# Kernel optimization log

Hardware: AMD Instinct MI355X
Metric: run time of the kernel (lower is better)

The kernel has to match this reference:

```python
import jax, jax.numpy as jnp
import numpy as np

HIDDEN = 1024
INTER = 2048
NUM_EXPERTS = 8
TOP_K = 2
GROUP_SIZE = 128
TOKENS = 4096


def _dequant_int4(packed, scale, group_size):
    # packed: [E, N, K//2] ints in [0,256) holding two uint4 nibbles (low | high<<4)
    # scale:  [E, N, K//group_size] float32
    E, N, Kh = packed.shape
    K = 2 * Kh
    low = packed & 0xF
    high = (packed >> 4) & 0xF
    # interleave: even K positions = low nibble, odd = high nibble
    q = jnp.stack([low, high], axis=-1).reshape(E, N, K) - 8  # int4 values in [-8,7]
    q = q.astype(jnp.float32).reshape(E, N, K // group_size, group_size)
    w = q * scale[..., None]
    return w.reshape(E, N, K)


def setup_inputs() -> dict:
    key = jax.random.key(0)
    k1, k2, k3, k4, k5, k6 = jax.random.split(key, 6)
    x = jax.random.normal(k1, (TOKENS, HIDDEN), dtype=jnp.float32)
    router_w = jax.random.normal(k2, (NUM_EXPERTS, HIDDEN), dtype=jnp.float32) * 0.02
    w1 = jax.random.randint(k3, (NUM_EXPERTS, 2 * INTER, HIDDEN // 2), 0, 256, dtype=jnp.int32)
    w1_scale = jax.random.uniform(k4, (NUM_EXPERTS, 2 * INTER, HIDDEN // GROUP_SIZE), dtype=jnp.float32) * 0.05
    w2 = jax.random.randint(k5, (NUM_EXPERTS, HIDDEN, INTER // 2), 0, 256, dtype=jnp.int32)
    w2_scale = jax.random.uniform(k6, (NUM_EXPERTS, HIDDEN, INTER // GROUP_SIZE), dtype=jnp.float32) * 0.05
    return {"x": x, "router_w": router_w, "w1": w1, "w1_scale": w1_scale, "w2": w2, "w2_scale": w2_scale}


def reference(x, router_w, w1, w1_scale, w2, w2_scale):
    # Router: topk then softmax over the top-k logits
    scores = x @ router_w.T                                 # [T, E]
    top_w, top_i = jax.lax.top_k(scores, TOP_K)             # [T, K]
    top_w = jax.nn.softmax(top_w, axis=-1).astype(jnp.float32)

    # Dequantize int4 grouped weights once
    w1_deq = _dequant_int4(w1, w1_scale, GROUP_SIZE)        # [E, 2I, H]
    w2_deq = _dequant_int4(w2, w2_scale, GROUP_SIZE)        # [E, H, I]

    out = jnp.zeros_like(x)
    for e in range(NUM_EXPERTS):
        # per-token routing weight for expert e (0 if not routed)
        ge = jnp.sum(top_w * (top_i == e), axis=-1)         # [T]
        h = x @ w1_deq[e].T                                  # [T, 2I]
        gate, up = h[:, :INTER], h[:, INTER:]
        a = jax.nn.silu(gate) * up                           # SwiGLU
        y = a @ w2_deq[e].T                                  # [T, H]
        out = out + ge[:, None] * y
    return out
```

## Files before the change

kernel.cpp:

```cpp
#include <hip/hip_runtime.h>
#include <hip/hip_bf16.h>

#define HIDDEN 1024
#define INTER 2048
#define NE 8
#define GS 128
#define TOKENS 4096
#define MAXROWS 9216
#define MAXTILES 72

typedef __bf16 bf16x8 __attribute__((ext_vector_type(8)));
typedef float f32x4 __attribute__((ext_vector_type(4)));

#define OFF_TOPKI 0u
#define OFF_TOPKW 32768u
#define OFF_CTRL  65536u
#define OFF_TOK   66048u
#define OFF_SLOT  102912u
#define OFF_TILE  135680u
#define OFF_XB    139776u
#define OFF_A     8530432u
#define OFF_W1D   46279168u
#define OFF_W2D   113388032u
#define OFF_Y0    OFF_W1D

__device__ __forceinline__ unsigned short f2bf(float f) {
  union { float f; unsigned int u; } v; v.f = f;
  unsigned int r = (v.u + 0x7FFFu + ((v.u >> 16) & 1u)) >> 16;
  return (unsigned short)r;
}
__device__ __forceinline__ float bf2f(unsigned int u) {
  union { unsigned int u; float f; } v; v.u = u << 16;
  return v.f;
}
__device__ __forceinline__ unsigned int pack2(unsigned short lo, unsigned short hi) {
  return (unsigned int)lo | ((unsigned int)hi << 16);
}

typedef const __attribute__((address_space(1))) unsigned int GAS;
typedef __attribute__((address_space(3))) unsigned int LAS;
__device__ __forceinline__ void gload16(const unsigned short* g, unsigned short* l) {
  __builtin_amdgcn_global_load_lds((GAS*)g, (LAS*)l, 16, 0, 0);
}


__global__ __launch_bounds__(256) void k_prep(const float* __restrict__ x,
    const float* __restrict__ rw, int* __restrict__ topki, float* __restrict__ topkw,
    const int* __restrict__ w1, const float* __restrict__ w1s,
    unsigned short* __restrict__ w1f,
    const int* __restrict__ w2, const float* __restrict__ w2s,
    unsigned short* __restrict__ w2f, unsigned short* __restrict__ xb) {
  int bid = blockIdx.x, tid = threadIdx.x;
  if (bid == 25600) {
    uint2 z; z.x = 0u; z.y = 0u;
    *reinterpret_cast<uint2*>(xb + (size_t)TOKENS * HIDDEN + tid * 4) = z;
    return;
  }
  if (bid >= 17408) {
    int gid = (bid - 17408) * 256 + tid;
    int lane = gid & 63, kt = (gid >> 6) & 63, ntP = (gid >> 12) & 63, e = gid >> 18;
    int n = ntP * 16 + (lane & 15), q = lane >> 4;
    size_t R = (size_t)e * 1024 + n;
    float s = w2s[R * 16 + (kt >> 2)];
    int4 p = *reinterpret_cast<const int4*>(w2 + R * 1024 + kt * 16 + q * 4);
    int pv[4] = { p.x, p.y, p.z, p.w };
    uint4 o; unsigned int ov[4];
#pragma unroll
    for (int j = 0; j < 4; j++) {
      float lo = (float)((pv[j] & 15) - 8) * s;
      float hi = (float)(((pv[j] >> 4) & 15) - 8) * s;
      ov[j] = pack2(f2bf(lo), f2bf(hi));
    }
    o.x = ov[0]; o.y = ov[1]; o.z = ov[2]; o.w = ov[3];
    *reinterpret_cast<uint4*>(w2f + (size_t)gid * 8) = o;
    return;
  }
  if (bid >= 1024) {
    int gid = (bid - 1024) * 256 + tid;
    int lane = gid & 63, kt = (gid >> 6) & 31, ntP = (gid >> 11) & 255, e = gid >> 19;
    int n = ntP * 16 + (lane & 15), q = lane >> 4;
    size_t R = (size_t)e * 4096 + n;
    float s = w1s[R * 8 + (kt >> 2)];
    int4 p = *reinterpret_cast<const int4*>(w1 + R * 512 + kt * 16 + q * 4);
    int pv[4] = { p.x, p.y, p.z, p.w };
    uint4 o; unsigned int ov[4];
#pragma unroll
    for (int j = 0; j < 4; j++) {
      float lo = (float)((pv[j] & 15) - 8) * s;
      float hi = (float)(((pv[j] >> 4) & 15) - 8) * s;
      ov[j] = pack2(f2bf(lo), f2bf(hi));
    }
    o.x = ov[0]; o.y = ov[1]; o.z = ov[2]; o.w = ov[3];
    *reinterpret_cast<uint4*>(w1f + (size_t)gid * 8) = o;
    return;
  }
  int wave = tid >> 6, lane = tid & 63;
  int t = bid * 4 + wave;
  float acc[NE];
#pragma unroll
  for (int e = 0; e < NE; e++) acc[e] = 0.f;
  const float* xr = x + (size_t)t * HIDDEN;
  unsigned short* xbr = xb + (size_t)t * HIDDEN;
  for (int i = lane; i < HIDDEN; i += 64) {
    float xv = xr[i];
    xbr[i] = f2bf(xv);
#pragma unroll
    for (int e = 0; e < NE; e++) acc[e] += xv * rw[e * HIDDEN + i];
  }
#pragma unroll
  for (int e = 0; e < NE; e++) {
    float v = acc[e];
    for (int off = 32; off > 0; off >>= 1) v += __shfl_down(v, off, 64);
    acc[e] = v;
  }
  if (lane == 0) {
    int b0 = 0; float s0 = acc[0];
#pragma unroll
    for (int e = 1; e < NE; e++) if (acc[e] > s0) { s0 = acc[e]; b0 = e; }
    int b1 = -1; float s1 = -3.0e38f;
#pragma unroll
    for (int e = 0; e < NE; e++) if (e != b0 && acc[e] > s1) { s1 = acc[e]; b1 = e; }
    float w0 = 1.f / (1.f + __expf(s1 - s0));
    topki[t * 2] = b0; topki[t * 2 + 1] = b1;
    topkw[t * 2] = w0; topkw[t * 2 + 1] = 1.f - w0;
  }
}

__global__ __launch_bounds__(256) void k_route2(const int* __restrict__ topki,
    int* __restrict__ ctrl, int* __restrict__ tok, int* __restrict__ slots,
    int* __restrict__ tilemap) {
  __shared__ int h[NE], off[NE], cnt[NE];
  int tid = threadIdx.x;
  if (tid < NE) h[tid] = 0;
  __syncthreads();
  for (int i = tid; i < TOKENS * 2; i += 256) atomicAdd(&h[topki[i]], 1);
  __syncthreads();
  if (tid == 0) {
    int run = 0, t = 0;
    for (int e = 0; e < NE; e++) {
      int c = h[e];
      ctrl[e] = c; ctrl[16 + e] = run; off[e] = run;
      int pc = (c + 127) & ~127;
      for (int mt = 0; mt < (pc >> 7); mt++) tilemap[t++] = (e << 20) | (run + mt * 128);
      run += pc;
    }
    ctrl[24] = run; ctrl[25] = t;
  }
  __syncthreads();
#pragma unroll
  for (int e = 0; e < NE; e++) {
    int c = h[e], pc = (c + 127) & ~127;
    for (int i = c + tid; i < pc; i += 256) tok[off[e] + i] = -1;
  }
  if (tid < NE) cnt[tid] = off[tid];
  __syncthreads();
  for (int i = tid; i < TOKENS * 2; i += 256) {
    int e = topki[i];
    int p = atomicAdd(&cnt[e], 1);
    tok[p] = i >> 1;
    slots[i] = p;
  }
}

__global__ __launch_bounds__(256) void k_gemm1(
    const unsigned short* __restrict__ xb, const unsigned short* __restrict__ w1f,
    const int* __restrict__ ctrl, const int* __restrict__ tilemap,
    const int* __restrict__ tok, unsigned short* __restrict__ a_f) {
  __shared__ unsigned short sA[128 * 32];
  int bid = blockIdx.x, tid = threadIdx.x;
  int nt = bid & 31, tile = bid >> 5;
  if (tile >= ctrl[25]) return;
  int tm = tilemap[tile];
  int e = tm >> 20, row0 = tm & 0xFFFFF;
  int wave = tid >> 6, lane = tid & 63;
  int ln = lane & 15, quad = lane >> 4;
  int wr = (wave & 1) * 64, wc = (wave >> 1) * 32;

  int srow = tid >> 2, scblk = tid & 3;
  int scol = (scblk ^ ((srow >> 1) & 3)) * 8;
  int t0 = tok[row0 + srow];
  int t1 = tok[row0 + 64 + srow];
  const unsigned short* gA0 = xb + (size_t)(t0 < 0 ? TOKENS : t0) * HIDDEN + scol;
  const unsigned short* gA1 = xb + (size_t)(t1 < 0 ? TOKENS : t1) * HIDDEN + scol;
  unsigned short* lA0 = sA + tid * 8;
  unsigned short* lA1 = sA + 64 * 32 + tid * 8;

  int ntPg = nt * 4 + (wave >> 1) * 2;
  const unsigned short* pbg0 = w1f + (size_t)(e * 256 + ntPg) * 16384 + lane * 8;
  const unsigned short* pbg1 = w1f + (size_t)(e * 256 + ntPg + 1) * 16384 + lane * 8;
  const unsigned short* pbu0 = w1f + (size_t)(e * 256 + 128 + ntPg) * 16384 + lane * 8;
  const unsigned short* pbu1 = w1f + (size_t)(e * 256 + 128 + ntPg + 1) * 16384 + lane * 8;

  bf16x8 bgc[2], buc[2];
  bgc[0] = *reinterpret_cast<const bf16x8*>(pbg0);
  bgc[1] = *reinterpret_cast<const bf16x8*>(pbg1);
  buc[0] = *reinterpret_cast<const bf16x8*>(pbu0);
  buc[1] = *reinterpret_cast<const bf16x8*>(pbu1);

  f32x4 aG[4][2] = {}, aU[4][2] = {};
#pragma unroll 2
  for (int kt = 0; kt < 32; kt++) {
    __syncthreads();
    gload16(gA0 + kt * 32, lA0);
    gload16(gA1 + kt * 32, lA1);
    __syncthreads();
    int o = (kt < 31) ? (kt + 1) * 512 : 0;
    bf16x8 bgn0 = *reinterpret_cast<const bf16x8*>(pbg0 + o);
    bf16x8 bgn1 = *reinterpret_cast<const bf16x8*>(pbg1 + o);
    bf16x8 bun0 = *reinterpret_cast<const bf16x8*>(pbu0 + o);
    bf16x8 bun1 = *reinterpret_cast<const bf16x8*>(pbu1 + o);
    bf16x8 af[4];
#pragma unroll
    for (int m = 0; m < 4; m++) {
      int ar = wr + m * 16 + ln;
      af[m] = *reinterpret_cast<const bf16x8*>(&sA[ar * 32 + (quad ^ ((ar >> 1) & 3)) * 8]);
    }
#pragma unroll
    for (int m = 0; m < 4; m++) {
      aG[m][0] = __builtin_amdgcn_mfma_f32_16x16x32_bf16(af[m], bgc[0], aG[m][0], 0, 0, 0);
      aG[m][1] = __builtin_amdgcn_mfma_f32_16x16x32_bf16(af[m], bgc[1], aG[m][1], 0, 0, 0);
      aU[m][0] = __builtin_amdgcn_mfma_f32_16x16x32_bf16(af[m], buc[0], aU[m][0], 0, 0, 0);
      aU[m][1] = __builtin_amdgcn_mfma_f32_16x16x32_bf16(af[m], buc[1], aU[m][1], 0, 0, 0);
    }
    bgc[0] = bgn0; bgc[1] = bgn1; buc[0] = bun0; buc[1] = bun1;
  }
#pragma unroll
  for (int m = 0; m < 4; m++)
#pragma unroll
    for (int n = 0; n < 2; n++) {
      int c = nt * 64 + wc + n * 16 + ln;
      int kta = c >> 5, qa = (c >> 3) & 3, ja = c & 7;
#pragma unroll
      for (int r = 0; r < 4; r++) {
        float g = aG[m][n][r], u = aU[m][n][r];
        float act = (g / (1.f + __expf(-g))) * u;
        int row = row0 + wr + m * 16 + quad * 4 + r;
        size_t idx = ((size_t)((row >> 4) * 64 + kta) * 64 + qa * 16 + (row & 15)) * 8 + ja;
        a_f[idx] = f2bf(act);
      }
    }
}

__global__ __launch_bounds__(256) void k_gemm2(
    const unsigned short* __restrict__ a_f, const unsigned short* __restrict__ w2f,
    const int* __restrict__ ctrl, const int* __restrict__ tilemap,
    unsigned short* __restrict__ y) {
  int bid = blockIdx.x, tid = threadIdx.x;
  int kp = bid & 1, nt = (bid >> 1) & 7, tile = bid >> 4;
  if (tile >= ctrl[25]) return;
  int tm = tilemap[tile];
  int e = tm >> 20, row0 = tm & 0xFFFFF;
  int n0 = nt * 128;
  int wave = tid >> 6, lane = tid & 63;
  int ln = lane & 15, quad = lane >> 4;
  int wr = (wave & 1) * 64, wc = (wave >> 1) * 64;

  int rt0 = (row0 >> 4) + (wave & 1) * 4;
  int ntP0 = nt * 8 + (wave >> 1) * 4;
  const unsigned short* pa[4];
  const unsigned short* pb[4];
#pragma unroll
  for (int m = 0; m < 4; m++)
    pa[m] = a_f + ((size_t)(rt0 + m) * 64 + kp * 32) * 512 + lane * 8;
#pragma unroll
  for (int n = 0; n < 4; n++)
    pb[n] = w2f + ((size_t)(e * 64 + ntP0 + n) * 64 + kp * 32) * 512 + lane * 8;

  bf16x8 ac[4], bc[4];
#pragma unroll
  for (int m = 0; m < 4; m++) ac[m] = *reinterpret_cast<const bf16x8*>(pa[m]);
#pragma unroll
  for (int n = 0; n < 4; n++) bc[n] = *reinterpret_cast<const bf16x8*>(pb[n]);

  f32x4 acc[4][4] = {};
#pragma unroll 2
  for (int i = 0; i < 32; i++) {
    int o = (i < 31) ? (i + 1) * 512 : 0;
    bf16x8 an[4], bn[4];
#pragma unroll
    for (int m = 0; m < 4; m++) an[m] = *reinterpret_cast<const bf16x8*>(pa[m] + o);
#pragma unroll
    for (int n = 0; n < 4; n++) bn[n] = *reinterpret_cast<const bf16x8*>(pb[n] + o);
#pragma unroll
    for (int m = 0; m < 4; m++)
#pragma unroll
      for (int n = 0; n < 4; n++)
        acc[m][n] = __builtin_amdgcn_mfma_f32_16x16x32_bf16(ac[m], bc[n], acc[m][n], 0, 0, 0);
#pragma unroll
    for (int m = 0; m < 4; m++) ac[m] = an[m];
#pragma unroll
    for (int n = 0; n < 4; n++) bc[n] = bn[n];
  }
  unsigned short* yk = y + (size_t)kp * MAXROWS * HIDDEN;
#pragma unroll
  for (int m = 0; m < 4; m++)
#pragma unroll
    for (int n = 0; n < 4; n++) {
      int col = n0 + wc + n * 16 + ln;
#pragma unroll
      for (int r = 0; r < 4; r++) {
        int row = row0 + wr + m * 16 + quad * 4 + r;
        yk[(size_t)row * HIDDEN + col] = f2bf(acc[m][n][r]);
      }
    }
}

__global__ __launch_bounds__(256) void k_combine(const unsigned short* __restrict__ y,
    const int* __restrict__ slots, const float* __restrict__ topkw,
    float* __restrict__ out) {
  int t = blockIdx.x;
  int c = threadIdx.x * 4;
  int s0 = slots[t * 2], s1 = slots[t * 2 + 1];
  float g0 = topkw[t * 2], g1 = topkw[t * 2 + 1];
  const unsigned short* y1 = y + (size_t)MAXROWS * HIDDEN;
  uint2 a0 = *reinterpret_cast<const uint2*>(y  + (size_t)s0 * HIDDEN + c);
  uint2 a1 = *reinterpret_cast<const uint2*>(y1 + (size_t)s0 * HIDDEN + c);
  uint2 b0 = *reinterpret_cast<const uint2*>(y  + (size_t)s1 * HIDDEN + c);
  uint2 b1 = *reinterpret_cast<const uint2*>(y1 + (size_t)s1 * HIDDEN + c);
  float4 o;
  o.x = g0 * (bf2f(a0.x & 0xffffu) + bf2f(a1.x & 0xffffu))
      + g1 * (bf2f(b0.x & 0xffffu) + bf2f(b1.x & 0xffffu));
  o.y = g0 * (bf2f(a0.x >> 16) + bf2f(a1.x >> 16))
      + g1 * (bf2f(b0.x >> 16) + bf2f(b1.x >> 16));
  o.z = g0 * (bf2f(a0.y & 0xffffu) + bf2f(a1.y & 0xffffu))
      + g1 * (bf2f(b0.y & 0xffffu) + bf2f(b1.y & 0xffffu));
  o.w = g0 * (bf2f(a0.y >> 16) + bf2f(a1.y >> 16))
      + g1 * (bf2f(b0.y >> 16) + bf2f(b1.y >> 16));
  *reinterpret_cast<float4*>(out + (size_t)t * HIDDEN + c) = o;
}

extern "C" void kernel_launch(void* const* d_in, const int* in_sizes, int n_in,
                              void* d_out, int out_size, void* d_ws, size_t ws_size,
                              hipStream_t stream) {
  const float* x   = (const float*)d_in[0];
  const float* rw  = (const float*)d_in[1];
  const int*   w1  = (const int*)d_in[2];
  const float* w1s = (const float*)d_in[3];
  const int*   w2  = (const int*)d_in[4];
  const float* w2s = (const float*)d_in[5];
  float* out = (float*)d_out;
  char* ws = (char*)d_ws;

  int*   topki = (int*)(ws + OFF_TOPKI);
  float* topkw = (float*)(ws + OFF_TOPKW);
  int*   ctrl  = (int*)(ws + OFF_CTRL);
  int*   tok   = (int*)(ws + OFF_TOK);
  int*   slots = (int*)(ws + OFF_SLOT);
  int*   tilemap = (int*)(ws + OFF_TILE);
  unsigned short* xb  = (unsigned short*)(ws + OFF_XB);
  unsigned short* a_f = (unsigned short*)(ws + OFF_A);
  unsigned short* w1f = (unsigned short*)(ws + OFF_W1D);
  unsigned short* w2f = (unsigned short*)(ws + OFF_W2D);
  unsigned short* y   = (unsigned short*)(ws + OFF_Y0);

  k_prep<<<25601, 256, 0, stream>>>(x, rw, topki, topkw, w1, w1s, w1f, w2, w2s, w2f, xb);
  k_route2<<<1, 256, 0, stream>>>(topki, ctrl, tok, slots, tilemap);
  k_gemm1<<<32 * MAXTILES, 256, 0, stream>>>(xb, w1f, ctrl, tilemap, tok, a_f);
  k_gemm2<<<16 * MAXTILES, 256, 0, stream>>>(a_f, w2f, ctrl, tilemap, y);
  k_combine<<<TOKENS, 256, 0, stream>>>(y, slots, topkw, out);
}
```

Baseline: 351.5 us.

## Stage gemm1 weights through LDS from row-major dequantized layout

The w1 dequant now writes a plain row-major [E, 2I, H] bf16 array with fully coalesced reads, instead of the MFMA-fragment-packed layout. gemm1 loads gate and up weight tiles into swizzled shared memory with global_load_lds, alongside the activation tile, and reads the B fragments from LDS. This removes the per-lane register prefetch of B fragments. It adds LDS traffic and loses the overlap of next-iteration weight loads with the MFMAs, since the loop is now fully synchronous with no double buffering.

```diff
diff --git a/kernel.cpp b/kernel.cpp
--- a/kernel.cpp
+++ b/kernel.cpp
@@ -47,7 +47,7 @@
 __global__ __launch_bounds__(256) void k_prep(const float* __restrict__ x,
     const float* __restrict__ rw, int* __restrict__ topki, float* __restrict__ topkw,
     const int* __restrict__ w1, const float* __restrict__ w1s,
-    unsigned short* __restrict__ w1f,
+    unsigned short* __restrict__ w1d,
     const int* __restrict__ w2, const float* __restrict__ w2s,
     unsigned short* __restrict__ w2f, unsigned short* __restrict__ xb) {
   int bid = blockIdx.x, tid = threadIdx.x;
@@ -77,11 +77,11 @@
   }
   if (bid >= 1024) {
     int gid = (bid - 1024) * 256 + tid;
-    int lane = gid & 63, kt = (gid >> 6) & 31, ntP = (gid >> 11) & 255, e = gid >> 19;
-    int n = ntP * 16 + (lane & 15), q = lane >> 4;
-    size_t R = (size_t)e * 4096 + n;
-    float s = w1s[R * 8 + (kt >> 2)];
-    int4 p = *reinterpret_cast<const int4*>(w1 + R * 512 + kt * 16 + q * 4);
+    int i4 = gid * 4;
+    int r = i4 >> 9;
+    int i = i4 & 511;
+    float s = w1s[r * 8 + (i >> 6)];
+    int4 p = *reinterpret_cast<const int4*>(w1 + (size_t)i4);
     int pv[4] = { p.x, p.y, p.z, p.w };
     uint4 o; unsigned int ov[4];
 #pragma unroll
@@ -91,7 +91,7 @@
       ov[j] = pack2(f2bf(lo), f2bf(hi));
     }
     o.x = ov[0]; o.y = ov[1]; o.z = ov[2]; o.w = ov[3];
-    *reinterpret_cast<uint4*>(w1f + (size_t)gid * 8) = o;
+    *reinterpret_cast<uint4*>(w1d + ((size_t)r << 10) + 2 * i) = o;
     return;
   }
   int wave = tid >> 6, lane = tid & 63;
@@ -163,15 +163,18 @@
 }
 
 __global__ __launch_bounds__(256) void k_gemm1(
-    const unsigned short* __restrict__ xb, const unsigned short* __restrict__ w1f,
+    const unsigned short* __restrict__ xb, const unsigned short* __restrict__ w1d,
     const int* __restrict__ ctrl, const int* __restrict__ tilemap,
     const int* __restrict__ tok, unsigned short* __restrict__ a_f) {
   __shared__ unsigned short sA[128 * 32];
+  __shared__ unsigned short sBg[64 * 32];
+  __shared__ unsigned short sBu[64 * 32];
   int bid = blockIdx.x, tid = threadIdx.x;
   int nt = bid & 31, tile = bid >> 5;
   if (tile >= ctrl[25]) return;
   int tm = tilemap[tile];
   int e = tm >> 20, row0 = tm & 0xFFFFF;
+  int n0 = nt * 64;
   int wave = tid >> 6, lane = tid & 63;
   int ln = lane & 15, quad = lane >> 4;
   int wr = (wave & 1) * 64, wc = (wave >> 1) * 32;
@@ -182,53 +185,47 @@
   int t1 = tok[row0 + 64 + srow];
   const unsigned short* gA0 = xb + (size_t)(t0 < 0 ? TOKENS : t0) * HIDDEN + scol;
   const unsigned short* gA1 = xb + (size_t)(t1 < 0 ? TOKENS : t1) * HIDDEN + scol;
+  const unsigned short* gBg = w1d + ((size_t)e * 4096 + n0 + srow) * HIDDEN + scol;
+  const unsigned short* gBu = gBg + (size_t)INTER * HIDDEN;
   unsigned short* lA0 = sA + tid * 8;
   unsigned short* lA1 = sA + 64 * 32 + tid * 8;
-
-  int ntPg = nt * 4 + (wave >> 1) * 2;
-  const unsigned short* pbg0 = w1f + (size_t)(e * 256 + ntPg) * 16384 + lane * 8;
-  const unsigned short* pbg1 = w1f + (size_t)(e * 256 + ntPg + 1) * 16384 + lane * 8;
-  const unsigned short* pbu0 = w1f + (size_t)(e * 256 + 128 + ntPg) * 16384 + lane * 8;
-  const unsigned short* pbu1 = w1f + (size_t)(e * 256 + 128 + ntPg + 1) * 16384 + lane * 8;
-
-  bf16x8 bgc[2], buc[2];
-  bgc[0] = *reinterpret_cast<const bf16x8*>(pbg0);
-  bgc[1] = *reinterpret_cast<const bf16x8*>(pbg1);
-  buc[0] = *reinterpret_cast<const bf16x8*>(pbu0);
-  buc[1] = *reinterpret_cast<const bf16x8*>(pbu1);
+  unsigned short* lBg = sBg + tid * 8;
+  unsigned short* lBu = sBu + tid * 8;
 
   f32x4 aG[4][2] = {}, aU[4][2] = {};
-#pragma unroll 2
-  for (int kt = 0; kt < 32; kt++) {
+  for (int k0 = 0; k0 < HIDDEN; k0 += 32) {
     __syncthreads();
-    gload16(gA0 + kt * 32, lA0);
-    gload16(gA1 + kt * 32, lA1);
+    gload16(gA0 + k0, lA0);
+    gload16(gA1 + k0, lA1);
+    gload16(gBg + k0, lBg);
+    gload16(gBu + k0, lBu);
     __syncthreads();
-    int o = (kt < 31) ? (kt + 1) * 512 : 0;
-    bf16x8 bgn0 = *reinterpret_cast<const bf16x8*>(pbg0 + o);
-    bf16x8 bgn1 = *reinterpret_cast<const bf16x8*>(pbg1 + o);
-    bf16x8 bun0 = *reinterpret_cast<const bf16x8*>(pbu0 + o);
-    bf16x8 bun1 = *reinterpret_cast<const bf16x8*>(pbu1 + o);
-    bf16x8 af[4];
+    bf16x8 af[4], bg[2], bu[2];
 #pragma unroll
     for (int m = 0; m < 4; m++) {
       int ar = wr + m * 16 + ln;
       af[m] = *reinterpret_cast<const bf16x8*>(&sA[ar * 32 + (quad ^ ((ar >> 1) & 3)) * 8]);
     }
 #pragma unroll
-    for (int m = 0; m < 4; m++) {
-      aG[m][0] = __builtin_amdgcn_mfma_f32_16x16x32_bf16(af[m], bgc[0], aG[m][0], 0, 0, 0);
-      aG[m][1] = __builtin_amdgcn_mfma_f32_16x16x32_bf16(af[m], bgc[1], aG[m][1], 0, 0, 0);
-      aU[m][0] = __builtin_amdgcn_mfma_f32_16x16x32_bf16(af[m], buc[0], aU[m][0], 0, 0, 0);
-      aU[m][1] = __builtin_amdgcn_mfma_f32_16x16x32_bf16(af[m], buc[1], aU[m][1], 0, 0, 0);
-    }
-    bgc[0] = bgn0; bgc[1] = bgn1; buc[0] = bun0; buc[1] = bun1;
+    for (int n = 0; n < 2; n++) {
+      int br = wc + n * 16 + ln;
+      int bo = br * 32 + (quad ^ ((br >> 1) & 3)) * 8;
+      bg[n] = *reinterpret_cast<const bf16x8*>(&sBg[bo]);
+      bu[n] = *reinterpret_cast<const bf16x8*>(&sBu[bo]);
+    }
+#pragma unroll
+    for (int m = 0; m < 4; m++)
+#pragma unroll
+      for (int n = 0; n < 2; n++) {
+        aG[m][n] = __builtin_amdgcn_mfma_f32_16x16x32_bf16(af[m], bg[n], aG[m][n], 0, 0, 0);
+        aU[m][n] = __builtin_amdgcn_mfma_f32_16x16x32_bf16(af[m], bu[n], aU[m][n], 0, 0, 0);
+      }
   }
 #pragma unroll
   for (int m = 0; m < 4; m++)
 #pragma unroll
     for (int n = 0; n < 2; n++) {
-      int c = nt * 64 + wc + n * 16 + ln;
+      int c = n0 + wc + n * 16 + ln;
       int kta = c >> 5, qa = (c >> 3) & 3, ja = c & 7;
 #pragma unroll
       for (int r = 0; r < 4; r++) {
@@ -349,13 +346,13 @@
   int*   tilemap = (int*)(ws + OFF_TILE);
   unsigned short* xb  = (unsigned short*)(ws + OFF_XB);
   unsigned short* a_f = (unsigned short*)(ws + OFF_A);
-  unsigned short* w1f = (unsigned short*)(ws + OFF_W1D);
+  unsigned short* w1d = (unsigned short*)(ws + OFF_W1D);
   unsigned short* w2f = (unsigned short*)(ws + OFF_W2D);
   unsigned short* y   = (unsigned short*)(ws + OFF_Y0);
 
-  k_prep<<<25601, 256, 0, stream>>>(x, rw, topki, topkw, w1, w1s, w1f, w2, w2s, w2f, xb);
+  k_prep<<<25601, 256, 0, stream>>>(x, rw, topki, topkw, w1, w1s, w1d, w2, w2s, w2f, xb);
   k_route2<<<1, 256, 0, stream>>>(topki, ctrl, tok, slots, tilemap);
-  k_gemm1<<<32 * MAXTILES, 256, 0, stream>>>(xb, w1f, ctrl, tilemap, tok, a_f);
+  k_gemm1<<<32 * MAXTILES, 256, 0, stream>>>(xb, w1d, ctrl, tilemap, tok, a_f);
   k_gemm2<<<16 * MAXTILES, 256, 0, stream>>>(a_f, w2f, ctrl, tilemap, y);
   k_combine<<<TOKENS, 256, 0, stream>>>(y, slots, topkw, out);
 }
```

Result: faster. 328.5 us (-6.5%).
